# Optimization experiments

Measured on AMD Instinct MI355X. Metric: run time of the kernel, lower is better.

Reference implementation:

```python
import jax, jax.numpy as jnp
import numpy as np

W_CD = 1.0   # cfg TRAIN.LOSS_WEIGHT_CHAMFER_DISTANCE
W_RV = 1.0   # cfg TRAIN.LOSS_WEIGHT_RANGE_VIEW
W_MASK = 1.0 # cfg TRAIN.LOSS_WEIGHT_MASK


def setup_inputs() -> dict:
    key = jax.random.key(0)
    k0, k1, k2, k3, k4 = jax.random.split(key, 5)
    B, T, H, W = 2, 5, 64, 2048   # batch, future steps, range-image dims
    N = M = 4096                  # n_samples (TEST.N_DOWNSAMPLED_POINTS_CD)
    output_rv = jax.random.normal(k0, (B, T, H, W), jnp.float32)
    mask_logits = jax.random.normal(k1, (B, T, H, W), jnp.float32)
    target_range_image = jax.random.normal(k2, (B, T, H, W), jnp.float32)
    output_points = jax.random.normal(k3, (B, T, N, 3), jnp.float32)
    target_points = jax.random.normal(k4, (B, T, M, 3), jnp.float32)
    return {
        "output_rv": output_rv,
        "mask_logits": mask_logits,
        "output_points": output_points,
        "target_points": target_points,
        "target_range_image": target_range_image,
    }


def _chamfer(output_points, target_points):
    on = jnp.sum(output_points * output_points, axis=-1)            # [B,T,N]
    tn = jnp.sum(target_points * target_points, axis=-1)            # [B,T,M]
    cross = jnp.einsum('btnd,btmd->btnm', output_points, target_points)
    d2 = on[..., :, None] + tn[..., None, :] - 2.0 * cross          # [B,T,N,M]
    dist1 = jnp.min(d2, axis=-1).mean(axis=-1)                      # [B,T] out->tgt NN
    dist2 = jnp.min(d2, axis=-2).mean(axis=-1)                      # [B,T] tgt->out NN
    cd_bt = dist1 + dist2                                           # per (b,s) CD
    return cd_bt.T, jnp.mean(cd_bt)                                 # [T,B] tensor, scalar mean


def reference(output_rv, mask_logits, output_points, target_points, target_range_image):
    # L1 range loss: output values are forced to -1 wherever target == -1
    out_m = jnp.where(target_range_image == -1.0, -1.0, output_rv)
    loss_rv = jnp.mean(jnp.abs(out_m - target_range_image))
    # mask BCE-with-logits: target mask is 1 where range view is valid (> 0)
    tmask = (target_range_image > 0.0).astype(output_rv.dtype)
    x = mask_logits
    loss_mask = jnp.mean(jnp.maximum(x, 0.0) - x * tmask + jnp.log1p(jnp.exp(-jnp.abs(x))))
    # Chamfer distance over fixed-size subsampled point clouds
    cd_tensor, loss_cd = _chamfer(output_points, target_points)
    total = W_CD * loss_cd + W_RV * loss_rv + W_MASK * loss_mask
    return total, cd_tensor, loss_cd, loss_rv, loss_mask
```

## Files before the change

### kernel.cpp

```cpp
#include <hip/hip_runtime.h>
#include <math.h>

#define BB 2
#define TT 5
#define NPTS 4096
#define NBT (BB * TT)
#define NELEM (BB * TT * 64 * 2048)

#define EW_BLOCKS 640
#define CH_BLOCKS 1280
#define QPB 64
#define NQC 64

#define EW1 1280
#define EW2 1920

typedef _Float16 h8 __attribute__((ext_vector_type(8)));
typedef float f32x16 __attribute__((ext_vector_type(16)));
typedef float f32x4 __attribute__((ext_vector_type(4)));

__device__ inline unsigned pkh(float a, float b) {
    union { _Float16 h[2]; unsigned u; } c;
    c.h[0] = (_Float16)a;
    c.h[1] = (_Float16)b;
    return c.u;
}

__global__ __launch_bounds__(256) void main_kernel(
        const float4* __restrict__ rv4,
        const float4* __restrict__ lg4,
        const float4* __restrict__ tg4,
        const float* __restrict__ OP,
        const float* __restrict__ TP,
        float* __restrict__ ws) {
    __shared__ __align__(16) uint2 pts[4096];
    __shared__ float nqlds[QPB];
    __shared__ float qmin[2][QPB];
    int bid = blockIdx.x;
    int tid = threadIdx.x;
    int lane = tid & 63;
    int wave = tid >> 6;

    if (bid < EW_BLOCKS) {
        float srv = 0.0f, smk = 0.0f;
        int base = (bid * 256 + tid) * 2;
#pragma unroll
        for (int u = 0; u < 2; ++u) {
            int i = base + u;
            float4 o4 = rv4[i];
            float4 x4 = lg4[i];
            float4 t4 = tg4[i];
            const float* op = &o4.x;
            const float* xp = &x4.x;
            const float* tp = &t4.x;
#pragma unroll
            for (int j = 0; j < 4; ++j) {
                float tv = tp[j];
                float ov = (tv == -1.0f) ? -1.0f : op[j];
                srv += fabsf(ov - tv);
                float tm = (tv > 0.0f) ? 1.0f : 0.0f;
                float xv = xp[j];
                smk += fmaxf(xv, 0.0f) - xv * tm + __logf(1.0f + __expf(-fabsf(xv)));
            }
        }
#pragma unroll
        for (int off = 32; off > 0; off >>= 1) {
            srv += __shfl_down(srv, off);
            smk += __shfl_down(smk, off);
        }
        __shared__ float s1[4], s2[4];
        if (lane == 0) { s1[wave] = srv; s2[wave] = smk; }
        __syncthreads();
        if (tid == 0) {
            ws[EW1 + bid] = s1[0] + s1[1] + s1[2] + s1[3];
            ws[EW2 + bid] = s2[0] + s2[1] + s2[2] + s2[3];
        }
        return;
    }

    int cb = bid - EW_BLOCKS;
    int dir = cb / (NBT * NQC);
    int rem = cb % (NBT * NQC);
    int bt = rem / NQC;
    int qc = rem % NQC;
    const float* P = dir ? TP : OP;
    const float* Q = dir ? OP : TP;
    const float* Pb = P + (size_t)bt * NPTS * 3;
    const float* Qb = Q + (size_t)bt * NPTS * 3;

    int qrow = lane & 31;
    int wq = wave & 1;
    int ph = wave >> 1;

    int qidx = qc * QPB + wq * 32 + qrow;
    float qx = 0.0f, qy = 0.0f, qz = 0.0f;
    if (lane < 32) {
        const float* p = Pb + (size_t)qidx * 3;
        qx = p[0]; qy = p[1]; qz = p[2];
        nqlds[wq * 32 + qrow] = fmaf(qx, qx, fmaf(qy, qy, qz * qz));
    }
    union { unsigned u[4]; h8 h; } ua;
    ua.u[0] = ua.u[1] = ua.u[2] = ua.u[3] = 0u;
    if (lane < 32) {
        ua.u[0] = pkh(-2.0f * qx, -2.0f * qy);
        ua.u[1] = pkh(-2.0f * qz, 1.0f);
    }
    h8 afrag = ua.h;

#pragma unroll
    for (int t = 0; t < 4; ++t) {
        int pt0 = t * 1024 + tid * 4;
        const f32x4* src = (const f32x4*)(Qb + (size_t)pt0 * 3);
        f32x4 c0 = src[0], c1 = src[1], c2 = src[2];
        float x0 = c0[0], y0 = c0[1], z0 = c0[2];
        float x1 = c0[3], y1 = c1[0], z1 = c1[1];
        float x2 = c1[2], y2 = c1[3], z2 = c2[0];
        float x3 = c2[1], y3 = c2[2], z3 = c2[3];
        float n0 = fmaf(x0, x0, fmaf(y0, y0, z0 * z0));
        float n1 = fmaf(x1, x1, fmaf(y1, y1, z1 * z1));
        float n2 = fmaf(x2, x2, fmaf(y2, y2, z2 * z2));
        float n3 = fmaf(x3, x3, fmaf(y3, y3, z3 * z3));
        uint4* dst = (uint4*)&pts[t * 1024 + tid * 4];
        dst[0] = make_uint4(pkh(x0, y0), pkh(z0, n0), pkh(x1, y1), pkh(z1, n1));
        dst[1] = make_uint4(pkh(x2, y2), pkh(z2, n2), pkh(x3, y3), pkh(z3, n3));
    }
    __syncthreads();

    const f32x16 zc = {0.0f, 0.0f, 0.0f, 0.0f, 0.0f, 0.0f, 0.0f, 0.0f,
                       0.0f, 0.0f, 0.0f, 0.0f, 0.0f, 0.0f, 0.0f, 0.0f};
    float vm[16];
#pragma unroll
    for (int r = 0; r < 16; ++r) vm[r] = INFINITY;

    const uint2* pb = pts + ph * 2048;
#pragma unroll 4
    for (int g = 0; g < 16; ++g) {
        uint2 b0 = pb[g * 128 + 0 * 32 + qrow];
        uint2 b1 = pb[g * 128 + 1 * 32 + qrow];
        uint2 b2 = pb[g * 128 + 2 * 32 + qrow];
        uint2 b3 = pb[g * 128 + 3 * 32 + qrow];
        union { unsigned u[4]; h8 h; } ub0, ub1, ub2, ub3;
        ub0.u[0] = b0.x; ub0.u[1] = b0.y; ub0.u[2] = 0u; ub0.u[3] = 0u;
        ub1.u[0] = b1.x; ub1.u[1] = b1.y; ub1.u[2] = 0u; ub1.u[3] = 0u;
        ub2.u[0] = b2.x; ub2.u[1] = b2.y; ub2.u[2] = 0u; ub2.u[3] = 0u;
        ub3.u[0] = b3.x; ub3.u[1] = b3.y; ub3.u[2] = 0u; ub3.u[3] = 0u;
        f32x16 d0 = __builtin_amdgcn_mfma_f32_32x32x16_f16(afrag, ub0.h, zc, 0, 0, 0);
        f32x16 d1 = __builtin_amdgcn_mfma_f32_32x32x16_f16(afrag, ub1.h, zc, 0, 0, 0);
        f32x16 d2 = __builtin_amdgcn_mfma_f32_32x32x16_f16(afrag, ub2.h, zc, 0, 0, 0);
        f32x16 d3 = __builtin_amdgcn_mfma_f32_32x32x16_f16(afrag, ub3.h, zc, 0, 0, 0);
#pragma unroll
        for (int r = 0; r < 16; ++r) {
            float a = d0[r], c = d1[r];
            asm("v_min3_f32 %0, %0, %1, %2" : "+v"(vm[r]) : "v"(a), "v"(c));
        }
#pragma unroll
        for (int r = 0; r < 16; ++r) {
            float a = d2[r], c = d3[r];
            asm("v_min3_f32 %0, %0, %1, %2" : "+v"(vm[r]) : "v"(a), "v"(c));
        }
    }

#pragma unroll
    for (int r = 0; r < 16; ++r) {
        float m = vm[r];
        m = fminf(m, __shfl_xor(m, 1));
        m = fminf(m, __shfl_xor(m, 2));
        m = fminf(m, __shfl_xor(m, 4));
        m = fminf(m, __shfl_xor(m, 8));
        m = fminf(m, __shfl_xor(m, 16));
        vm[r] = m;
    }
    if ((lane & 31) == 0) {
        int half = lane >> 5;
#pragma unroll
        for (int r = 0; r < 16; ++r) {
            int row = (r & 3) + 8 * (r >> 2) + 4 * half;
            qmin[ph][wq * 32 + row] = vm[r];
        }
    }
    __syncthreads();

    if (wave == 0) {
        float m = fminf(qmin[0][lane], qmin[1][lane]) + nqlds[lane];
#pragma unroll
        for (int off = 32; off > 0; off >>= 1) m += __shfl_down(m, off);
        if (lane == 0) ws[cb] = m;
    }
}

__global__ void finalize_kernel(const float* __restrict__ ws, float* __restrict__ out) {
    __shared__ float grp[20];
    __shared__ float ra[4], rb[4];
    int tid = threadIdx.x;
    int lane = tid & 63;
    int wave = tid >> 6;

    for (int g = wave; g < 20; g += 4) {
        float s = ws[g * 64 + lane];
#pragma unroll
        for (int off = 32; off > 0; off >>= 1) s += __shfl_down(s, off);
        if (lane == 0) grp[g] = s;
    }

    float sa = 0.0f, sb = 0.0f;
    for (int i = tid; i < EW_BLOCKS; i += 256) {
        sa += ws[EW1 + i];
        sb += ws[EW2 + i];
    }
#pragma unroll
    for (int off = 32; off > 0; off >>= 1) {
        sa += __shfl_down(sa, off);
        sb += __shfl_down(sb, off);
    }
    if (lane == 0) { ra[wave] = sa; rb[wave] = sb; }
    __syncthreads();

    if (tid == 0) {
        const float inv_e = 1.0f / (float)NELEM;
        float loss_rv = (ra[0] + ra[1] + ra[2] + ra[3]) * inv_e;
        float loss_mask = (rb[0] + rb[1] + rb[2] + rb[3]) * inv_e;
        float cd_sum = 0.0f;
        for (int bt = 0; bt < NBT; ++bt) {
            float cd = (grp[bt] + grp[NBT + bt]) * (1.0f / NPTS);
            int b = bt / TT;
            int t = bt % TT;
            out[1 + t * BB + b] = cd;
            cd_sum += cd;
        }
        float loss_cd = cd_sum / (float)NBT;
        out[0] = loss_cd + loss_rv + loss_mask;
        out[11] = loss_cd;
        out[12] = loss_rv;
        out[13] = loss_mask;
    }
}

extern "C" void kernel_launch(void* const* d_in, const int* in_sizes, int n_in,
                              void* d_out, int out_size, void* d_ws, size_t ws_size,
                              hipStream_t stream) {
    const float* output_rv = (const float*)d_in[0];
    const float* mask_logits = (const float*)d_in[1];
    const float* output_points = (const float*)d_in[2];
    const float* target_points = (const float*)d_in[3];
    const float* target_rv = (const float*)d_in[4];
    float* out = (float*)d_out;
    float* ws = (float*)d_ws;

    main_kernel<<<EW_BLOCKS + CH_BLOCKS, 256, 0, stream>>>(
        (const float4*)output_rv, (const float4*)mask_logits,
        (const float4*)target_rv, output_points, target_points, ws);

    finalize_kernel<<<1, 256, 0, stream>>>(ws, out);
}
```

Before: 30.56 us.

## Reuse LDS point fragments across two query tiles per wave and reorder blocks

After: 32.64 us. +6.8%, slower.

```diff
diff --git a/kernel.cpp b/kernel.cpp
--- a/kernel.cpp
+++ b/kernel.cpp
@@ -7,22 +7,21 @@
 #define NBT (BB * TT)
 #define NELEM (BB * TT * 64 * 2048)
 
+#define CH_BLOCKS 1280
+#define NQC 64
 #define EW_BLOCKS 640
-#define CH_BLOCKS 1280
-#define QPB 64
-#define NQC 64
 
 #define EW1 1280
 #define EW2 1920
 
 typedef _Float16 h8 __attribute__((ext_vector_type(8)));
+typedef __fp16 fp16x2 __attribute__((ext_vector_type(2)));
 typedef float f32x16 __attribute__((ext_vector_type(16)));
 typedef float f32x4 __attribute__((ext_vector_type(4)));
 
-__device__ inline unsigned pkh(float a, float b) {
-    union { _Float16 h[2]; unsigned u; } c;
-    c.h[0] = (_Float16)a;
-    c.h[1] = (_Float16)b;
+__device__ inline unsigned pk2(float a, float b) {
+    union { fp16x2 h; unsigned u; } c;
+    c.h = __builtin_amdgcn_cvt_pkrtz(a, b);
     return c.u;
 }
 
@@ -34,16 +33,17 @@
         const float* __restrict__ TP,
         float* __restrict__ ws) {
     __shared__ __align__(16) uint2 pts[4096];
-    __shared__ float nqlds[QPB];
-    __shared__ float qmin[2][QPB];
+    __shared__ float nqlds[64];
+    __shared__ float qmin[4][64];
     int bid = blockIdx.x;
     int tid = threadIdx.x;
     int lane = tid & 63;
     int wave = tid >> 6;
 
-    if (bid < EW_BLOCKS) {
+    if (bid >= CH_BLOCKS) {
+        int eb = bid - CH_BLOCKS;
         float srv = 0.0f, smk = 0.0f;
-        int base = (bid * 256 + tid) * 2;
+        int base = (eb * 256 + tid) * 2;
 #pragma unroll
         for (int u = 0; u < 2; ++u) {
             int i = base + u;
@@ -72,15 +72,14 @@
         if (lane == 0) { s1[wave] = srv; s2[wave] = smk; }
         __syncthreads();
         if (tid == 0) {
-            ws[EW1 + bid] = s1[0] + s1[1] + s1[2] + s1[3];
-            ws[EW2 + bid] = s2[0] + s2[1] + s2[2] + s2[3];
+            ws[EW1 + eb] = s1[0] + s1[1] + s1[2] + s1[3];
+            ws[EW2 + eb] = s2[0] + s2[1] + s2[2] + s2[3];
         }
         return;
     }
 
-    int cb = bid - EW_BLOCKS;
-    int dir = cb / (NBT * NQC);
-    int rem = cb % (NBT * NQC);
+    int dir = bid / (NBT * NQC);
+    int rem = bid % (NBT * NQC);
     int bt = rem / NQC;
     int qc = rem % NQC;
     const float* P = dir ? TP : OP;
@@ -89,23 +88,24 @@
     const float* Qb = Q + (size_t)bt * NPTS * 3;
 
     int qrow = lane & 31;
-    int wq = wave & 1;
-    int ph = wave >> 1;
-
-    int qidx = qc * QPB + wq * 32 + qrow;
-    float qx = 0.0f, qy = 0.0f, qz = 0.0f;
+
+    int qbase = qc * 64 + qrow;
+    const float* pL = Pb + (size_t)qbase * 3;
+    const float* pH = pL + 32 * 3;
+    float lx = pL[0], ly = pL[1], lz = pL[2];
+    float hx = pH[0], hy = pH[1], hz = pH[2];
+    nqlds[qrow] = fmaf(lx, lx, fmaf(ly, ly, lz * lz));
+    nqlds[32 + qrow] = fmaf(hx, hx, fmaf(hy, hy, hz * hz));
+    union { unsigned u[4]; h8 h; } uaL, uaH;
+    uaL.u[0] = uaL.u[1] = uaL.u[2] = uaL.u[3] = 0u;
+    uaH.u[0] = uaH.u[1] = uaH.u[2] = uaH.u[3] = 0u;
     if (lane < 32) {
-        const float* p = Pb + (size_t)qidx * 3;
-        qx = p[0]; qy = p[1]; qz = p[2];
-        nqlds[wq * 32 + qrow] = fmaf(qx, qx, fmaf(qy, qy, qz * qz));
-    }
-    union { unsigned u[4]; h8 h; } ua;
-    ua.u[0] = ua.u[1] = ua.u[2] = ua.u[3] = 0u;
-    if (lane < 32) {
-        ua.u[0] = pkh(-2.0f * qx, -2.0f * qy);
-        ua.u[1] = pkh(-2.0f * qz, 1.0f);
-    }
-    h8 afrag = ua.h;
+        uaL.u[0] = pk2(-2.0f * lx, -2.0f * ly);
+        uaL.u[1] = pk2(-2.0f * lz, 1.0f);
+        uaH.u[0] = pk2(-2.0f * hx, -2.0f * hy);
+        uaH.u[1] = pk2(-2.0f * hz, 1.0f);
+    }
+    h8 aL = uaL.h, aH = uaH.h;
 
 #pragma unroll
     for (int t = 0; t < 4; ++t) {
@@ -121,70 +121,73 @@
         float n2 = fmaf(x2, x2, fmaf(y2, y2, z2 * z2));
         float n3 = fmaf(x3, x3, fmaf(y3, y3, z3 * z3));
         uint4* dst = (uint4*)&pts[t * 1024 + tid * 4];
-        dst[0] = make_uint4(pkh(x0, y0), pkh(z0, n0), pkh(x1, y1), pkh(z1, n1));
-        dst[1] = make_uint4(pkh(x2, y2), pkh(z2, n2), pkh(x3, y3), pkh(z3, n3));
+        dst[0] = make_uint4(pk2(x0, y0), pk2(z0, n0), pk2(x1, y1), pk2(z1, n1));
+        dst[1] = make_uint4(pk2(x2, y2), pk2(z2, n2), pk2(x3, y3), pk2(z3, n3));
     }
     __syncthreads();
 
     const f32x16 zc = {0.0f, 0.0f, 0.0f, 0.0f, 0.0f, 0.0f, 0.0f, 0.0f,
                        0.0f, 0.0f, 0.0f, 0.0f, 0.0f, 0.0f, 0.0f, 0.0f};
-    float vm[16];
-#pragma unroll
-    for (int r = 0; r < 16; ++r) vm[r] = INFINITY;
-
-    const uint2* pb = pts + ph * 2048;
+    float vmL[16], vmH[16];
+#pragma unroll
+    for (int r = 0; r < 16; ++r) { vmL[r] = INFINITY; vmH[r] = INFINITY; }
+
+    const uint2* pb = pts + wave * 1024;
 #pragma unroll 4
     for (int g = 0; g < 16; ++g) {
-        uint2 b0 = pb[g * 128 + 0 * 32 + qrow];
-        uint2 b1 = pb[g * 128 + 1 * 32 + qrow];
-        uint2 b2 = pb[g * 128 + 2 * 32 + qrow];
-        uint2 b3 = pb[g * 128 + 3 * 32 + qrow];
-        union { unsigned u[4]; h8 h; } ub0, ub1, ub2, ub3;
+        uint2 b0 = pb[g * 64 + qrow];
+        uint2 b1 = pb[g * 64 + 32 + qrow];
+        union { unsigned u[4]; h8 h; } ub0, ub1;
         ub0.u[0] = b0.x; ub0.u[1] = b0.y; ub0.u[2] = 0u; ub0.u[3] = 0u;
         ub1.u[0] = b1.x; ub1.u[1] = b1.y; ub1.u[2] = 0u; ub1.u[3] = 0u;
-        ub2.u[0] = b2.x; ub2.u[1] = b2.y; ub2.u[2] = 0u; ub2.u[3] = 0u;
-        ub3.u[0] = b3.x; ub3.u[1] = b3.y; ub3.u[2] = 0u; ub3.u[3] = 0u;
-        f32x16 d0 = __builtin_amdgcn_mfma_f32_32x32x16_f16(afrag, ub0.h, zc, 0, 0, 0);
-        f32x16 d1 = __builtin_amdgcn_mfma_f32_32x32x16_f16(afrag, ub1.h, zc, 0, 0, 0);
-        f32x16 d2 = __builtin_amdgcn_mfma_f32_32x32x16_f16(afrag, ub2.h, zc, 0, 0, 0);
-        f32x16 d3 = __builtin_amdgcn_mfma_f32_32x32x16_f16(afrag, ub3.h, zc, 0, 0, 0);
+        f32x16 dL0 = __builtin_amdgcn_mfma_f32_32x32x16_f16(aL, ub0.h, zc, 0, 0, 0);
+        f32x16 dL1 = __builtin_amdgcn_mfma_f32_32x32x16_f16(aL, ub1.h, zc, 0, 0, 0);
+        f32x16 dH0 = __builtin_amdgcn_mfma_f32_32x32x16_f16(aH, ub0.h, zc, 0, 0, 0);
+        f32x16 dH1 = __builtin_amdgcn_mfma_f32_32x32x16_f16(aH, ub1.h, zc, 0, 0, 0);
 #pragma unroll
         for (int r = 0; r < 16; ++r) {
-            float a = d0[r], c = d1[r];
-            asm("v_min3_f32 %0, %0, %1, %2" : "+v"(vm[r]) : "v"(a), "v"(c));
+            float a = dL0[r], c = dL1[r];
+            asm("v_min3_f32 %0, %0, %1, %2" : "+v"(vmL[r]) : "v"(a), "v"(c));
         }
 #pragma unroll
         for (int r = 0; r < 16; ++r) {
-            float a = d2[r], c = d3[r];
-            asm("v_min3_f32 %0, %0, %1, %2" : "+v"(vm[r]) : "v"(a), "v"(c));
+            float a = dH0[r], c = dH1[r];
+            asm("v_min3_f32 %0, %0, %1, %2" : "+v"(vmH[r]) : "v"(a), "v"(c));
         }
     }
 
 #pragma unroll
     for (int r = 0; r < 16; ++r) {
-        float m = vm[r];
-        m = fminf(m, __shfl_xor(m, 1));
-        m = fminf(m, __shfl_xor(m, 2));
-        m = fminf(m, __shfl_xor(m, 4));
-        m = fminf(m, __shfl_xor(m, 8));
-        m = fminf(m, __shfl_xor(m, 16));
-        vm[r] = m;
+        float mL = vmL[r], mH = vmH[r];
+        mL = fminf(mL, __shfl_xor(mL, 1));
+        mH = fminf(mH, __shfl_xor(mH, 1));
+        mL = fminf(mL, __shfl_xor(mL, 2));
+        mH = fminf(mH, __shfl_xor(mH, 2));
+        mL = fminf(mL, __shfl_xor(mL, 4));
+        mH = fminf(mH, __shfl_xor(mH, 4));
+        mL = fminf(mL, __shfl_xor(mL, 8));
+        mH = fminf(mH, __shfl_xor(mH, 8));
+        mL = fminf(mL, __shfl_xor(mL, 16));
+        mH = fminf(mH, __shfl_xor(mH, 16));
+        vmL[r] = mL; vmH[r] = mH;
     }
     if ((lane & 31) == 0) {
-        int half = lane >> 5;
+        int h4 = (lane >> 5) * 4;
 #pragma unroll
         for (int r = 0; r < 16; ++r) {
-            int row = (r & 3) + 8 * (r >> 2) + 4 * half;
-            qmin[ph][wq * 32 + row] = vm[r];
+            int row = (r & 3) + 8 * (r >> 2) + h4;
+            qmin[wave][row] = vmL[r];
+            qmin[wave][32 + row] = vmH[r];
         }
     }
     __syncthreads();
 
     if (wave == 0) {
-        float m = fminf(qmin[0][lane], qmin[1][lane]) + nqlds[lane];
+        float m = fminf(fminf(qmin[0][lane], qmin[1][lane]),
+                        fminf(qmin[2][lane], qmin[3][lane])) + nqlds[lane];
 #pragma unroll
         for (int off = 32; off > 0; off >>= 1) m += __shfl_down(m, off);
-        if (lane == 0) ws[cb] = m;
+        if (lane == 0) ws[bid] = m;
     }
 }
 
@@ -246,7 +249,7 @@
     float* out = (float*)d_out;
     float* ws = (float*)d_ws;
 
-    main_kernel<<<EW_BLOCKS + CH_BLOCKS, 256, 0, stream>>>(
+    main_kernel<<<CH_BLOCKS + EW_BLOCKS, 256, 0, stream>>>(
         (const float4*)output_rv, (const float4*)mask_logits,
         (const float4*)target_rv, output_points, target_points, ws);
 
```
